# Optimization experiments

Measured on AMD Instinct MI355X. Metric: run time of the kernel, lower is better.

## Reference

```python
import jax, jax.numpy as jnp
import numpy as np

N_LAYERS = 6
D_MODEL = 512
D_FFN = 2048
N_STATE = 64
KSIZE = 31
BATCH = 8
SEQ = 2048
IN_SIZE = 80


def _ln(x, g, b, eps=1e-5):
    m = jnp.mean(x, axis=-1, keepdims=True)
    v = jnp.mean((x - m) ** 2, axis=-1, keepdims=True)
    return (x - m) * jax.lax.rsqrt(v + eps) * g + b


def _ffn(x, g, b, w1, b1, w2, b2):
    # LayerNorm -> Linear(D->F) -> GELU -> Linear(F->D)  (PositionalwiseFeedForward)
    h = jax.nn.gelu(_ln(x, g, b) @ w1 + b1)
    return h @ w2 + b2


def _dss(x, lam_re, lam_im, c_re, c_im, d_skip, log_dt, w_out, b_out):
    # Diagonal state-space (DSS-EXP): generate length-T kernel from diagonal poles,
    # apply causal conv via FFT, skip D*u, GELU, GLU output projection.
    Bx, T, H = x.shape
    dt = jnp.exp(log_dt)
    lam = -jnp.exp(lam_re) + 1j * lam_im                        # [N] stable poles (Re<0)
    P = jnp.exp(lam[:, None] * (dt * jnp.arange(T))[None, :])   # [N, T]
    C = c_re + 1j * c_im                                        # [H, N]
    kern = jnp.einsum('hn,nt->ht', C, P).real * dt              # [H, T]
    u = x.transpose(0, 2, 1)                                    # [B, H, T]
    n = 2 * T
    y = jnp.fft.irfft(jnp.fft.rfft(u, n=n) * jnp.fft.rfft(kern, n=n), n=n)[..., :T]
    y = y + d_skip[None, :, None] * u
    y = jax.nn.gelu(y.transpose(0, 2, 1))                       # [B, T, H]
    z = y @ w_out + b_out                                       # [B, T, 2H]
    a, g = jnp.split(z, 2, axis=-1)
    return a * jax.nn.sigmoid(g)                                # GLU


def _conv_module(x, g1, b1, bw, bb, dw, db, g2, b2, lw, lb):
    # LN -> 1x1 conv to 2D + GLU -> depthwise conv (SAME, k=31) -> LN -> GELU -> Linear
    y = _ln(x, g1, b1)
    y = y @ bw.T + bb                                           # [B, T, 2D]
    a, g = jnp.split(y, 2, axis=-1)
    y = a * jax.nn.sigmoid(g)                                   # GLU over channels
    yc = y.transpose(0, 2, 1)                                   # [B, D, T]
    yc = jax.lax.conv_general_dilated(
        yc, dw[:, None, :], (1,), 'SAME',
        feature_group_count=yc.shape[1],
        dimension_numbers=('NCH', 'OIH', 'NCH'))
    yc = yc + db[None, :, None]
    y = jax.nn.gelu(_ln(yc.transpose(0, 2, 1), g2, b2))
    return y @ lw.T + lb


def _forward(src, speaker_embs, src_w, src_b,
             ffn1_ln_g, ffn1_ln_b, ffn1_w1, ffn1_b1, ffn1_w2, ffn1_b2,
             norm1_g, norm1_b,
             lam_re, lam_im, c_re, c_im, ssm_d, log_dt, dss_out_w, dss_out_b,
             conv_ln_g, conv_ln_b, bneck_w, bneck_b, dw_w, dw_b,
             conv_ln2_g, conv_ln2_b, conv_lin_w, conv_lin_b,
             ffn2_ln_g, ffn2_ln_b, ffn2_w1, ffn2_b1, ffn2_w2, ffn2_b2,
             norm2_g, norm2_b, final_g, final_b):
    x = src @ src_w + src_b                                     # custom_src_module Linear
    for i in range(N_LAYERS):
        x = x + 0.5 * _ffn(x, ffn1_ln_g[i], ffn1_ln_b[i], ffn1_w1[i], ffn1_b1[i], ffn1_w2[i], ffn1_b2[i])
        skip = x
        x = _ln(x, norm1_g[i], norm1_b[i])
        x = _dss(x, lam_re[i], lam_im[i], c_re[i], c_im[i], ssm_d[i], log_dt[i], dss_out_w[i], dss_out_b[i])
        x = x + skip
        x = x + _conv_module(x, conv_ln_g[i], conv_ln_b[i], bneck_w[i], bneck_b[i], dw_w[i], dw_b[i],
                             conv_ln2_g[i], conv_ln2_b[i], conv_lin_w[i], conv_lin_b[i])
        x = _ln(x + 0.5 * _ffn(x, ffn2_ln_g[i], ffn2_ln_b[i], ffn2_w1[i], ffn2_b1[i], ffn2_w2[i], ffn2_b2[i]),
                norm2_g[i], norm2_b[i])
    x = _ln(x, final_g, final_b, eps=1e-6)
    return x + speaker_embs


def setup_inputs() -> dict:
    key = jax.random.key(0)
    ks = iter(jax.random.split(key, 64))
    def rn(shape, s=0.02):
        return (jax.random.normal(next(ks), shape) * s).astype(jnp.float32)
    L, D, F, N, K = N_LAYERS, D_MODEL, D_FFN, N_STATE, KSIZE
    return dict(
        src=jax.random.normal(next(ks), (BATCH, SEQ, IN_SIZE), dtype=jnp.float32),
        speaker_embs=jax.random.normal(next(ks), (BATCH, 1, D), dtype=jnp.float32),
        src_w=rn((IN_SIZE, D)), src_b=jnp.zeros((D,), jnp.float32),
        ffn1_ln_g=jnp.ones((L, D), jnp.float32), ffn1_ln_b=jnp.zeros((L, D), jnp.float32),
        ffn1_w1=rn((L, D, F)), ffn1_b1=jnp.zeros((L, F), jnp.float32),
        ffn1_w2=rn((L, F, D)), ffn1_b2=jnp.zeros((L, D), jnp.float32),
        norm1_g=jnp.ones((L, D), jnp.float32), norm1_b=jnp.zeros((L, D), jnp.float32),
        lam_re=rn((L, N), 0.5), lam_im=rn((L, N), 3.0),
        c_re=rn((L, D, N), 0.1), c_im=rn((L, D, N), 0.1),
        ssm_d=rn((L, D), 1.0), log_dt=jnp.full((L,), float(np.log(0.01)), jnp.float32),
        dss_out_w=rn((L, D, 2 * D)), dss_out_b=jnp.zeros((L, 2 * D), jnp.float32),
        conv_ln_g=jnp.ones((L, D), jnp.float32), conv_ln_b=jnp.zeros((L, D), jnp.float32),
        bneck_w=rn((L, 2 * D, D)), bneck_b=jnp.zeros((L, 2 * D), jnp.float32),
        dw_w=rn((L, D, K), 0.1), dw_b=jnp.zeros((L, D), jnp.float32),
        conv_ln2_g=jnp.ones((L, D), jnp.float32), conv_ln2_b=jnp.zeros((L, D), jnp.float32),
        conv_lin_w=rn((L, D, D)), conv_lin_b=jnp.zeros((L, D), jnp.float32),
        ffn2_ln_g=jnp.ones((L, D), jnp.float32), ffn2_ln_b=jnp.zeros((L, D), jnp.float32),
        ffn2_w1=rn((L, D, F)), ffn2_b1=jnp.zeros((L, F), jnp.float32),
        ffn2_w2=rn((L, F, D)), ffn2_b2=jnp.zeros((L, D), jnp.float32),
        norm2_g=jnp.ones((L, D), jnp.float32), norm2_b=jnp.zeros((L, D), jnp.float32),
        final_g=jnp.ones((D,), jnp.float32), final_b=jnp.zeros((D,), jnp.float32),
    )


def reference(src, speaker_embs, src_w, src_b,
              ffn1_ln_g, ffn1_ln_b, ffn1_w1, ffn1_b1, ffn1_w2, ffn1_b2,
              norm1_g, norm1_b,
              lam_re, lam_im, c_re, c_im, ssm_d, log_dt, dss_out_w, dss_out_b,
              conv_ln_g, conv_ln_b, bneck_w, bneck_b, dw_w, dw_b,
              conv_ln2_g, conv_ln2_b, conv_lin_w, conv_lin_b,
              ffn2_ln_g, ffn2_ln_b, ffn2_w1, ffn2_b1, ffn2_w2, ffn2_b2,
              norm2_g, norm2_b, final_g, final_b):
    return _forward(src, speaker_embs, src_w, src_b,
                    ffn1_ln_g, ffn1_ln_b, ffn1_w1, ffn1_b1, ffn1_w2, ffn1_b2,
                    norm1_g, norm1_b,
                    lam_re, lam_im, c_re, c_im, ssm_d, log_dt, dss_out_w, dss_out_b,
                    conv_ln_g, conv_ln_b, bneck_w, bneck_b, dw_w, dw_b,
                    conv_ln2_g, conv_ln2_b, conv_lin_w, conv_lin_b,
                    ffn2_ln_g, ffn2_ln_b, ffn2_w1, ffn2_b1, ffn2_w2, ffn2_b2,
                    norm2_g, norm2_b, final_g, final_b)
```

## Files before the change

### kernel.cpp

```cpp
#include <hip/hip_runtime.h>
#include <hip/hip_bf16.h>
#include <stdint.h>


#define NL 6
#define TT 2048
#define BB 8
#define DD 512
#define FF 2048
#define ROWS (BB*TT)

typedef __attribute__((ext_vector_type(4))) float f32x4;
typedef __attribute__((ext_vector_type(8))) short s16x8;

#define DEVI __device__ __forceinline__

DEVI float bf2f(uint32_t u) { union { uint32_t i; float f; } v; v.i = u << 16; return v.f; }
DEVI uint16_t f2bf(float f) {
    union { float f; uint32_t i; } v; v.f = f;
    uint32_t x = v.i;
    return (uint16_t)((x + 0x7fffu + ((x >> 16) & 1u)) >> 16);
}
DEVI float gelu_f(float x) {
    float x2 = x * x;
    float z  = x * fmaf(x2, 0.07135481627f, 1.5957691216f);
    return x * __builtin_amdgcn_rcpf(1.0f + __expf(-z));
}
DEVI float sigm(float x) { return __builtin_amdgcn_rcpf(1.0f + __expf(-x)); }

DEVI void gload16(const uint16_t* g, uint16_t* l) {
    __builtin_amdgcn_global_load_lds((const __attribute__((address_space(1))) void*)g,
                                     (__attribute__((address_space(3))) void*)l, 16, 0, 0);
}

__global__ void k_wtrans(const float* __restrict__ src, uint16_t* __restrict__ dst,
                         int K, int N) {
    __shared__ float tile[32][33];
    int l = blockIdx.z;
    const float* s = src + (size_t)l * K * N;
    uint16_t*    d = dst + (size_t)l * N * K;
    int n0 = blockIdx.x * 32, k0 = blockIdx.y * 32;
    int tx = threadIdx.x, ty = threadIdx.y;
#pragma unroll
    for (int i = 0; i < 4; i++) {
        int k = k0 + ty + i * 8;
        tile[ty + i * 8][tx] = s[(size_t)k * N + n0 + tx];
    }
    __syncthreads();
#pragma unroll
    for (int i = 0; i < 4; i++) {
        int n = n0 + ty + i * 8;
        d[(size_t)n * K + k0 + tx] = f2bf(tile[tx][ty + i * 8]);
    }
}
__global__ void k_wcvt(const float* __restrict__ src, uint16_t* __restrict__ dst, int n) {
    int i = blockIdx.x * 256 + threadIdx.x;
    if (i < n) dst[i] = f2bf(src[i]);
}
__global__ void k_dwt(const float* __restrict__ dw, float* __restrict__ dwt) {
    int i = blockIdx.x * 256 + threadIdx.x;
    int tot = NL * DD * 31;
    if (i >= tot) return;
    int l = i / (DD * 31), r = i % (DD * 31), d = r / 31, k = r % 31;
    dwt[(size_t)l * 31 * DD + k * DD + d] = dw[i];
}
__global__ void k_srcpad(const float* __restrict__ src, uint16_t* __restrict__ dst) {
    int i = blockIdx.x * 256 + threadIdx.x;
    if (i >= ROWS * 128) return;
    int r = i >> 7, c = i & 127;
    dst[i] = (c < 80) ? f2bf(src[(size_t)r * 80 + c]) : (uint16_t)0;
}
__global__ void k_wsrcpad(const float* __restrict__ w, uint16_t* __restrict__ dst) {
    int i = blockIdx.x * 256 + threadIdx.x;
    if (i >= DD * 128) return;
    int n = i >> 7, k = i & 127;
    dst[i] = (k < 80) ? f2bf(w[(size_t)k * DD + n]) : (uint16_t)0;
}

template <int MODE>
__global__ void k_ln(const float* __restrict__ in, void* __restrict__ outp,
                     const float* __restrict__ gam, const float* __restrict__ bet,
                     const float* __restrict__ spk, float eps) {
    int row  = blockIdx.x * 4 + (threadIdx.x >> 6);
    int lane = threadIdx.x & 63;
    const float* x = in + (size_t)row * DD;
    float4 a0 = *(const float4*)&x[lane * 4];
    float4 a1 = *(const float4*)&x[256 + lane * 4];
    float v[8] = {a0.x, a0.y, a0.z, a0.w, a1.x, a1.y, a1.z, a1.w};
    float s = 0.f, q = 0.f;
#pragma unroll
    for (int i = 0; i < 8; i++) { s += v[i]; q += v[i] * v[i]; }
#pragma unroll
    for (int m = 1; m < 64; m <<= 1) { s += __shfl_xor(s, m); q += __shfl_xor(q, m); }
    float mean = s * (1.0f / 512.0f);
    float var  = fmaxf(q * (1.0f / 512.0f) - mean * mean, 0.0f);
    float inv  = rsqrtf(var + eps);
    float4 g0 = *(const float4*)&gam[lane * 4];
    float4 g1 = *(const float4*)&gam[256 + lane * 4];
    float4 b0 = *(const float4*)&bet[lane * 4];
    float4 b1 = *(const float4*)&bet[256 + lane * 4];
    float gv[8] = {g0.x, g0.y, g0.z, g0.w, g1.x, g1.y, g1.z, g1.w};
    float bv[8] = {b0.x, b0.y, b0.z, b0.w, b1.x, b1.y, b1.z, b1.w};
    float y[8];
#pragma unroll
    for (int i = 0; i < 8; i++) y[i] = (v[i] - mean) * inv * gv[i] + bv[i];
    uint16_t* o = (uint16_t*)outp + (size_t)row * DD;
    uint2 p0, p1;
    p0.x = (uint32_t)f2bf(y[0]) | ((uint32_t)f2bf(y[1]) << 16);
    p0.y = (uint32_t)f2bf(y[2]) | ((uint32_t)f2bf(y[3]) << 16);
    p1.x = (uint32_t)f2bf(y[4]) | ((uint32_t)f2bf(y[5]) << 16);
    p1.y = (uint32_t)f2bf(y[6]) | ((uint32_t)f2bf(y[7]) << 16);
    *(uint2*)&o[lane * 4]       = p0;
    *(uint2*)&o[256 + lane * 4] = p1;
}

template <int M2>
__global__ void k_ln2(const float* __restrict__ in, float* __restrict__ X,
                      void* __restrict__ out2,
                      const float* __restrict__ g1, const float* __restrict__ b1,
                      const float* __restrict__ g2, const float* __restrict__ b2,
                      const float* __restrict__ spk, float eps2) {
    int row  = blockIdx.x * 4 + (threadIdx.x >> 6);
    int lane = threadIdx.x & 63;
    const float* x = in + (size_t)row * DD;
    float4 a0 = *(const float4*)&x[lane * 4];
    float4 a1 = *(const float4*)&x[256 + lane * 4];
    float v[8] = {a0.x, a0.y, a0.z, a0.w, a1.x, a1.y, a1.z, a1.w};
    float s = 0.f, q = 0.f;
#pragma unroll
    for (int i = 0; i < 8; i++) { s += v[i]; q += v[i] * v[i]; }
#pragma unroll
    for (int m = 1; m < 64; m <<= 1) { s += __shfl_xor(s, m); q += __shfl_xor(q, m); }
    float mean = s * (1.0f / 512.0f);
    float var  = fmaxf(q * (1.0f / 512.0f) - mean * mean, 0.0f);
    float inv  = rsqrtf(var + 1e-5f);
    float4 g0 = *(const float4*)&g1[lane * 4];
    float4 g1v = *(const float4*)&g1[256 + lane * 4];
    float4 b0 = *(const float4*)&b1[lane * 4];
    float4 b1v = *(const float4*)&b1[256 + lane * 4];
    float gv[8] = {g0.x, g0.y, g0.z, g0.w, g1v.x, g1v.y, g1v.z, g1v.w};
    float bv[8] = {b0.x, b0.y, b0.z, b0.w, b1v.x, b1v.y, b1v.z, b1v.w};
    float y[8];
    float s2 = 0.f, q2 = 0.f;
#pragma unroll
    for (int i = 0; i < 8; i++) {
        y[i] = (v[i] - mean) * inv * gv[i] + bv[i];
        s2 += y[i]; q2 += y[i] * y[i];
    }
    if (M2 == 6) {
        float* xo = X + (size_t)row * DD;
        *(float4*)&xo[lane * 4]       = make_float4(y[0], y[1], y[2], y[3]);
        *(float4*)&xo[256 + lane * 4] = make_float4(y[4], y[5], y[6], y[7]);
    }
#pragma unroll
    for (int m = 1; m < 64; m <<= 1) { s2 += __shfl_xor(s2, m); q2 += __shfl_xor(q2, m); }
    float mean2 = s2 * (1.0f / 512.0f);
    float var2  = fmaxf(q2 * (1.0f / 512.0f) - mean2 * mean2, 0.0f);
    float inv2  = rsqrtf(var2 + eps2);
    float4 G0 = *(const float4*)&g2[lane * 4];
    float4 G1 = *(const float4*)&g2[256 + lane * 4];
    float4 B0 = *(const float4*)&b2[lane * 4];
    float4 B1v = *(const float4*)&b2[256 + lane * 4];
    float Gv[8] = {G0.x, G0.y, G0.z, G0.w, G1.x, G1.y, G1.z, G1.w};
    float Bv[8] = {B0.x, B0.y, B0.z, B0.w, B1v.x, B1v.y, B1v.z, B1v.w};
    float z[8];
#pragma unroll
    for (int i = 0; i < 8; i++) z[i] = (y[i] - mean2) * inv2 * Gv[i] + Bv[i];
    if (M2 == 6) {
        uint16_t* o = (uint16_t*)out2 + (size_t)row * DD;
        uint2 p0, p1;
        p0.x = (uint32_t)f2bf(z[0]) | ((uint32_t)f2bf(z[1]) << 16);
        p0.y = (uint32_t)f2bf(z[2]) | ((uint32_t)f2bf(z[3]) << 16);
        p1.x = (uint32_t)f2bf(z[4]) | ((uint32_t)f2bf(z[5]) << 16);
        p1.y = (uint32_t)f2bf(z[6]) | ((uint32_t)f2bf(z[7]) << 16);
        *(uint2*)&o[lane * 4]       = p0;
        *(uint2*)&o[256 + lane * 4] = p1;
    } else {
        const float* sp = spk + (size_t)(row >> 11) * DD;
        float4 s0 = *(const float4*)&sp[lane * 4];
        float4 s1 = *(const float4*)&sp[256 + lane * 4];
        float* o = (float*)out2 + (size_t)row * DD;
        *(float4*)&o[lane * 4]       = make_float4(z[0]+s0.x, z[1]+s0.y, z[2]+s0.z, z[3]+s0.w);
        *(float4*)&o[256 + lane * 4] = make_float4(z[4]+s1.x, z[5]+s1.y, z[6]+s1.z, z[7]+s1.w);
    }
}

__global__ void k_gluln(const uint16_t* __restrict__ H, float* __restrict__ X,
                        uint16_t* __restrict__ out,
                        const float* __restrict__ gam, const float* __restrict__ bet) {
    int row  = blockIdx.x * 4 + (threadIdx.x >> 6);
    int lane = threadIdx.x & 63;
    const uint16_t* hr = H + (size_t)row * 1024;
    uint2 ha0 = *(const uint2*)&hr[lane * 4];
    uint2 ha1 = *(const uint2*)&hr[256 + lane * 4];
    uint2 hg0 = *(const uint2*)&hr[512 + lane * 4];
    uint2 hg1 = *(const uint2*)&hr[768 + lane * 4];
    uint32_t aw[4] = {ha0.x, ha0.y, ha1.x, ha1.y};
    uint32_t gw[4] = {hg0.x, hg0.y, hg1.x, hg1.y};
    float* xr = X + (size_t)row * DD;
    float4 x0 = *(const float4*)&xr[lane * 4];
    float4 x1 = *(const float4*)&xr[256 + lane * 4];
    float xv[8] = {x0.x, x0.y, x0.z, x0.w, x1.x, x1.y, x1.z, x1.w};
    float v[8];
#pragma unroll
    for (int p = 0; p < 4; p++) {
        float a0 = bf2f(aw[p] & 0xffffu), a1 = bf2f(aw[p] >> 16);
        float g0 = bf2f(gw[p] & 0xffffu), g1 = bf2f(gw[p] >> 16);
        v[2*p]   = xv[2*p]   + a0 * sigm(g0);
        v[2*p+1] = xv[2*p+1] + a1 * sigm(g1);
    }
    *(float4*)&xr[lane * 4]       = make_float4(v[0], v[1], v[2], v[3]);
    *(float4*)&xr[256 + lane * 4] = make_float4(v[4], v[5], v[6], v[7]);
    float s = 0.f, q = 0.f;
#pragma unroll
    for (int i = 0; i < 8; i++) { s += v[i]; q += v[i] * v[i]; }
#pragma unroll
    for (int m = 1; m < 64; m <<= 1) { s += __shfl_xor(s, m); q += __shfl_xor(q, m); }
    float mean = s * (1.0f / 512.0f);
    float var  = fmaxf(q * (1.0f / 512.0f) - mean * mean, 0.0f);
    float inv  = rsqrtf(var + 1e-5f);
    float4 g0 = *(const float4*)&gam[lane * 4];
    float4 g1 = *(const float4*)&gam[256 + lane * 4];
    float4 b0 = *(const float4*)&bet[lane * 4];
    float4 b1 = *(const float4*)&bet[256 + lane * 4];
    float gv[8] = {g0.x, g0.y, g0.z, g0.w, g1.x, g1.y, g1.z, g1.w};
    float bv[8] = {b0.x, b0.y, b0.z, b0.w, b1.x, b1.y, b1.z, b1.w};
    uint16_t* o = out + (size_t)row * DD;
    uint2 p0, p1;
    float y0 = (v[0]-mean)*inv*gv[0]+bv[0], y1 = (v[1]-mean)*inv*gv[1]+bv[1];
    float y2 = (v[2]-mean)*inv*gv[2]+bv[2], y3 = (v[3]-mean)*inv*gv[3]+bv[3];
    float y4 = (v[4]-mean)*inv*gv[4]+bv[4], y5 = (v[5]-mean)*inv*gv[5]+bv[5];
    float y6 = (v[6]-mean)*inv*gv[6]+bv[6], y7 = (v[7]-mean)*inv*gv[7]+bv[7];
    p0.x = (uint32_t)f2bf(y0) | ((uint32_t)f2bf(y1) << 16);
    p0.y = (uint32_t)f2bf(y2) | ((uint32_t)f2bf(y3) << 16);
    p1.x = (uint32_t)f2bf(y4) | ((uint32_t)f2bf(y5) << 16);
    p1.y = (uint32_t)f2bf(y6) | ((uint32_t)f2bf(y7) << 16);
    *(uint2*)&o[lane * 4]       = p0;
    *(uint2*)&o[256 + lane * 4] = p1;
}

template <int MODE, int BN>
__global__ __launch_bounds__(512, 2) void k_gemm3(
    const uint16_t* __restrict__ A, const uint16_t* __restrict__ Bt,
    const float* __restrict__ bias, int M, int N, int K,
    void* __restrict__ outp, float* __restrict__ X) {
    constexpr int MR = 8;
    constexpr int NR = BN / 64;
    constexpr int ABLK = 16;
    constexpr int BBLK = BN / 16;
    constexpr int APW = 2;
    constexpr int BPW = BBLK / 8;
    constexpr int LV  = APW + BPW;
    __shared__ __align__(16) uint16_t As[3][ABLK * 512];
    __shared__ __align__(16) uint16_t Bs[3][BBLK * 512];
    int tid = threadIdx.x;
    int wave = tid >> 6, lane = tid & 63;
    int l15 = lane & 15, l16 = lane >> 4;
    int wr = wave >> 2, wc = wave & 3;

    int nwg = gridDim.x;
    int q8  = nwg >> 3;
    int wg  = (blockIdx.x & 7) * q8 + (blockIdx.x >> 3);
    int nbx = M >> 8;
    int bx = wg % nbx, by = wg / nbx;
    int m0 = bx * 256, n0 = by * BN;

    const uint16_t* srcA[APW];
    const uint16_t* srcB[BPW];
#pragma unroll
    for (int p = 0; p < APW; p++) {
        int bi = wave * APW + p;
        srcA[p] = A + (size_t)(m0 + bi * 16 + l15) * K + l16 * 8;
    }
#pragma unroll
    for (int p = 0; p < BPW; p++) {
        int bi = wave * BPW + p;
        srcB[p] = Bt + (size_t)(n0 + bi * 16 + l15) * K + l16 * 8;
    }

    f32x4 acc[MR][NR];
#pragma unroll
    for (int i = 0; i < MR; i++)
#pragma unroll
        for (int j = 0; j < NR; j++) acc[i][j] = (f32x4){0.f, 0.f, 0.f, 0.f};

    auto STAGE = [&](int tt) {
        int b = tt % 3;
        int kof = tt << 5;
#pragma unroll
        for (int p = 0; p < APW; p++)
            gload16(srcA[p] + kof, &As[b][(wave * APW + p) * 512]);
#pragma unroll
        for (int p = 0; p < BPW; p++)
            gload16(srcB[p] + kof, &Bs[b][(wave * BPW + p) * 512]);
    };

    int nk = K >> 5;
    STAGE(0);
    STAGE(1);
    for (int t = 0; t < nk; ++t) {
        if (t + 1 < nk) {
            if (LV == 4) asm volatile("s_waitcnt vmcnt(4)" ::: "memory");
            else         asm volatile("s_waitcnt vmcnt(3)" ::: "memory");
        } else {
            asm volatile("s_waitcnt vmcnt(0)" ::: "memory");
        }
        __builtin_amdgcn_s_barrier();
        asm volatile("" ::: "memory");
        if (t + 2 < nk) STAGE(t + 2);
        int buf = t % 3;
        s16x8 af[MR], bfr[NR];
#pragma unroll
        for (int i = 0; i < MR; i++)
            af[i] = *(const s16x8*)&As[buf][(wr * MR + i) * 512 + lane * 8];
#pragma unroll
        for (int j = 0; j < NR; j++)
            bfr[j] = *(const s16x8*)&Bs[buf][(wc * NR + j) * 512 + lane * 8];
#pragma unroll
        for (int i = 0; i < MR; i++)
#pragma unroll
            for (int j = 0; j < NR; j++)
                acc[i][j] = __builtin_amdgcn_mfma_f32_16x16x32_bf16(af[i], bfr[j], acc[i][j], 0, 0, 0);
    }
#pragma unroll
    for (int i = 0; i < MR; i++) {
#pragma unroll
        for (int j = 0; j < NR; j++) {
            int gcol = n0 + wc * NR * 16 + j * 16 + l15;
            float bv = bias[gcol];
#pragma unroll
            for (int q = 0; q < 4; q++) {
                int grow = m0 + wr * MR * 16 + i * 16 + l16 * 4 + q;
                float v = acc[i][j][q] + bv;
                if (MODE == 0) {
                    ((uint16_t*)outp)[(size_t)grow * N + gcol] = f2bf(gelu_f(v));
                } else if (MODE == 1) {
                    ((uint16_t*)outp)[(size_t)grow * N + gcol] = f2bf(v);
                } else if (MODE == 2) {
                    X[(size_t)grow * DD + gcol] += 0.5f * v;
                } else if (MODE == 3) {
                    X[(size_t)grow * DD + gcol] += v;
                } else if (MODE == 4) {
                    ((float*)outp)[(size_t)grow * DD + gcol] =
                        X[(size_t)grow * DD + gcol] + 0.5f * v;
                } else {
                    X[(size_t)grow * DD + gcol] = v;
                }
            }
        }
    }
}

__global__ void k_tpose(const uint16_t* __restrict__ in, uint16_t* __restrict__ out,
                        int R, int C) {
    __shared__ uint16_t tile[32][33];
    size_t boff = (size_t)blockIdx.z * R * C;
    int c0 = blockIdx.x * 32, r0 = blockIdx.y * 32;
    int tx = threadIdx.x, ty = threadIdx.y;
#pragma unroll
    for (int i = 0; i < 4; i++)
        tile[ty + i * 8][tx] = in[boff + (size_t)(r0 + ty + i * 8) * C + c0 + tx];
    __syncthreads();
#pragma unroll
    for (int i = 0; i < 4; i++)
        out[boff + (size_t)(c0 + ty + i * 8) * R + r0 + tx] = tile[tx][ty + i * 8];
}

__global__ __launch_bounds__(64) void k_phiprep(
        const float* __restrict__ lam_re, const float* __restrict__ lam_im,
        const float* __restrict__ log_dt, uint16_t* __restrict__ PHI,
        float* __restrict__ A64f) {
    int l = blockIdx.x, n = threadIdx.x;
    float dt = expf(log_dt[l]);
    float lr = lam_re[l * 64 + n], li = lam_im[l * 64 + n];
    float mag = expf(-expf(lr) * dt), th = li * dt;
    float Are = mag * __cosf(th), Aim = mag * __sinf(th);
    float Pre = 1.f, Pim = 0.f;
    uint16_t* ph = PHI + (size_t)l * 8192;
    for (int tau = 0; tau < 64; tau++) {
        int s = 63 - tau;
        ph[n * 64 + s]        = f2bf(Pre);
        ph[(64 + n) * 64 + s] = f2bf(Pim);
        float nr = Pre * Are - Pim * Aim;
        float ni = Pre * Aim + Pim * Are;
        Pre = nr; Pim = ni;
    }
    A64f[l * 128 + 2 * n]     = Pre;
    A64f[l * 128 + 2 * n + 1] = Pim;
}

__global__ __launch_bounds__(64) void k_gprep(
        const float* __restrict__ lam_re, const float* __restrict__ lam_im,
        const float* __restrict__ c_re, const float* __restrict__ c_im,
        const float* __restrict__ ssm_d, const float* __restrict__ log_dt,
        int l, uint16_t* __restrict__ G) {
    int h = blockIdx.x, n = threadIdx.x;
    __shared__ float klds[64];
    float dt = expf(log_dt[l]);
    float lr = lam_re[l * 64 + n], li = lam_im[l * 64 + n];
    float mag = expf(-expf(lr) * dt), th = li * dt;
    float Are = mag * __cosf(th), Aim = mag * __sinf(th);
    float Cre = c_re[(size_t)l * DD * 64 + h * 64 + n];
    float Cim = c_im[(size_t)l * DD * 64 + h * 64 + n];
    uint16_t* Gh = G + (size_t)h * 64 * 192;
    float Pre = 1.f, Pim = 0.f;
    for (int r = 0; r < 64; r++) {
        float t = Cre * Pre - Cim * Pim;
        float s = t;
        s += __shfl_xor(s, 1);  s += __shfl_xor(s, 2);  s += __shfl_xor(s, 4);
        s += __shfl_xor(s, 8);  s += __shfl_xor(s, 16); s += __shfl_xor(s, 32);
        if (n == 0) klds[r] = dt * s;
        float nr = Pre * Are - Pim * Aim;
        float ni = Pre * Aim + Pim * Are;
        float wre = dt * (Cre * nr - Cim * ni);
        float wim = dt * (Cre * ni + Cim * nr);
        Gh[r * 192 + 64 + n]  = f2bf(wre);
        Gh[r * 192 + 128 + n] = f2bf(-wim);
        Pre = nr; Pim = ni;
    }
    __syncthreads();
    float dh = ssm_d[l * DD + h];
    for (int r = 0; r < 64; r++) {
        int c = n;
        float val = (c < r) ? klds[r - c] : (c == r ? klds[0] + dh : 0.f);
        Gh[r * 192 + c] = f2bf(val);
    }
}

__global__ __launch_bounds__(256) void k_pass1(
        const uint16_t* __restrict__ u, const uint16_t* __restrict__ PHI,
        uint16_t* __restrict__ E) {
    __shared__ __align__(16) uint16_t Phs[128 * 72];
    int tid = threadIdx.x;
    for (int v = tid; v < 1024; v += 256) {
        int row = v >> 3, kb = v & 7;
        *(s16x8*)&Phs[row * 72 + kb * 8] = *(const s16x8*)&PHI[row * 64 + kb * 8];
    }
    __syncthreads();
    int wave = tid >> 6, lane = tid & 63;
    int l15 = lane & 15, l16 = lane >> 4;
    int m0 = (wave & 1) * 64;
    int colbase = blockIdx.x * 128 + (wave >> 1) * 64;
    f32x4 acc[4][4];
#pragma unroll
    for (int i = 0; i < 4; i++)
#pragma unroll
        for (int j = 0; j < 4; j++) acc[i][j] = (f32x4){0.f, 0.f, 0.f, 0.f};
#pragma unroll
    for (int kt = 0; kt < 64; kt += 32) {
        s16x8 a[4], b[4];
#pragma unroll
        for (int i = 0; i < 4; i++)
            a[i] = *(const s16x8*)&Phs[(m0 + i * 16 + l15) * 72 + kt + l16 * 8];
#pragma unroll
        for (int j = 0; j < 4; j++)
            b[j] = *(const s16x8*)(u + (size_t)(colbase + j * 16 + l15) * 64 + kt + l16 * 8);
#pragma unroll
        for (int i = 0; i < 4; i++)
#pragma unroll
            for (int j = 0; j < 4; j++)
                acc[i][j] = __builtin_amdgcn_mfma_f32_16x16x32_bf16(a[i], b[j], acc[i][j], 0, 0, 0);
    }
#pragma unroll
    for (int i = 0; i < 4; i++)
#pragma unroll
        for (int j = 0; j < 4; j++) {
            int col = colbase + j * 16 + l15;
            int r0  = m0 + i * 16 + l16 * 4;
            uint32_t p0 = (uint32_t)f2bf(acc[i][j][0]) | ((uint32_t)f2bf(acc[i][j][1]) << 16);
            uint32_t p1 = (uint32_t)f2bf(acc[i][j][2]) | ((uint32_t)f2bf(acc[i][j][3]) << 16);
            *(uint2*)&E[(size_t)col * 128 + r0] = make_uint2(p0, p1);
        }
}

__global__ void k_pass2(const uint16_t* __restrict__ E, const float* __restrict__ A64f,
                        int l, uint16_t* __restrict__ Sp) {
    int gid = blockIdx.x * 256 + threadIdx.x;
    int n = gid & 63, bh = gid >> 6;
    int b = bh >> 9, h = bh & 511;
    float2 A = *(const float2*)&A64f[l * 128 + 2 * n];
    float Sre = 0.f, Sim = 0.f;
    const uint16_t* Eb = E + (size_t)bh * 32 * 128;
    uint16_t* So = Sp + (size_t)h * 32768 + (size_t)b * 32 * 128;
    for (int i = 0; i < 32; i++) {
        So[i * 128 + n]      = f2bf(Sre);
        So[i * 128 + 64 + n] = f2bf(Sim);
        float er = bf2f((uint32_t)Eb[i * 128 + n]);
        float ei = bf2f((uint32_t)Eb[i * 128 + 64 + n]);
        float nr = A.x * Sre - A.y * Sim + er;
        float ni = A.x * Sim + A.y * Sre + ei;
        Sre = nr; Sim = ni;
    }
}

__global__ __launch_bounds__(256) void k_pass3(
        const uint16_t* __restrict__ G, const uint16_t* __restrict__ u,
        const uint16_t* __restrict__ Sp, uint16_t* __restrict__ Y) {
    __shared__ __align__(16) uint16_t Gs[64 * 200];
    int h = blockIdx.x, tid = threadIdx.x;
    for (int v = tid; v < 1536; v += 256) {
        int row = v / 24, kb = v % 24;
        *(s16x8*)&Gs[row * 200 + kb * 8] = *(const s16x8*)&G[(size_t)h * 12288 + row * 192 + kb * 8];
    }
    __syncthreads();
    int wave = tid >> 6, lane = tid & 63;
    int l15 = lane & 15, l16 = lane >> 4;
    int wn = wave * 64;
    const uint16_t* uh = u + (size_t)h * TT;
    const uint16_t* sh = Sp + (size_t)h * 32768;
    f32x4 acc[4][4];
#pragma unroll
    for (int i = 0; i < 4; i++)
#pragma unroll
        for (int j = 0; j < 4; j++) acc[i][j] = (f32x4){0.f, 0.f, 0.f, 0.f};
#pragma unroll
    for (int kt = 0; kt < 192; kt += 32) {
        s16x8 a[4], b[4];
#pragma unroll
        for (int i = 0; i < 4; i++)
            a[i] = *(const s16x8*)&Gs[(i * 16 + l15) * 200 + kt + l16 * 8];
#pragma unroll
        for (int j = 0; j < 4; j++) {
            int col = wn + j * 16 + l15;
            const uint16_t* src;
            if (kt < 64)
                src = uh + (size_t)(col >> 5) * (DD * TT) + (col & 31) * 64 + kt + l16 * 8;
            else
                src = sh + (size_t)col * 128 + (kt - 64) + l16 * 8;
            b[j] = *(const s16x8*)src;
        }
#pragma unroll
        for (int i = 0; i < 4; i++)
#pragma unroll
            for (int j = 0; j < 4; j++)
                acc[i][j] = __builtin_amdgcn_mfma_f32_16x16x32_bf16(a[i], b[j], acc[i][j], 0, 0, 0);
    }
#pragma unroll
    for (int i = 0; i < 4; i++)
#pragma unroll
        for (int j = 0; j < 4; j++) {
            int col = wn + j * 16 + l15;
            int r0  = i * 16 + l16 * 4;
            uint16_t* dst = Y + (size_t)(col >> 5) * (DD * TT) + (size_t)h * TT + (col & 31) * 64 + r0;
            uint32_t p0 = (uint32_t)f2bf(acc[i][j][0]) | ((uint32_t)f2bf(acc[i][j][1]) << 16);
            uint32_t p1 = (uint32_t)f2bf(acc[i][j][2]) | ((uint32_t)f2bf(acc[i][j][3]) << 16);
            *(uint2*)&dst[0] = make_uint2(p0, p1);
        }
}

__global__ void k_tgelu(const uint16_t* __restrict__ y, uint16_t* __restrict__ out) {
    __shared__ uint16_t tile[32][33];
    int b = blockIdx.z;
    int t0 = blockIdx.x * 32, h0 = blockIdx.y * 32;
    int tx = threadIdx.x, ty = threadIdx.y;
    const uint16_t* yb = y + (size_t)b * DD * TT;
#pragma unroll
    for (int i = 0; i < 4; i++) {
        int h = h0 + ty + i * 8;
        tile[ty + i * 8][tx] = f2bf(gelu_f(bf2f((uint32_t)yb[(size_t)h * TT + t0 + tx])));
    }
    __syncthreads();
    uint16_t* ob = out + (size_t)b * TT * DD;
#pragma unroll
    for (int i = 0; i < 4; i++) {
        int t = t0 + ty + i * 8;
        ob[(size_t)t * DD + h0 + tx] = tile[tx][ty + i * 8];
    }
}

__global__ void k_glu(const uint16_t* __restrict__ z, uint16_t* __restrict__ out) {
    int i = blockIdx.x * 256 + threadIdx.x;
    int r = i >> 8;
    int c = (i & 255) * 2;
    uint32_t av = *(const uint32_t*)&z[(size_t)r * 1024 + c];
    uint32_t gv = *(const uint32_t*)&z[(size_t)r * 1024 + 512 + c];
    float a0 = bf2f(av & 0xffffu), a1 = bf2f(av >> 16);
    float g0 = bf2f(gv & 0xffffu), g1 = bf2f(gv >> 16);
    float v0 = a0 * sigm(g0), v1 = a1 * sigm(g1);
    uint32_t p = (uint32_t)f2bf(v0) | ((uint32_t)f2bf(v1) << 16);
    *(uint32_t*)&out[(size_t)r * DD + c] = p;
}

__global__ __launch_bounds__(256) void k_dwln(
        const uint16_t* __restrict__ in, const float* __restrict__ dwt,
        const float* __restrict__ db, const float* __restrict__ gam,
        const float* __restrict__ bet, uint16_t* __restrict__ out) {
    __shared__ __align__(16) uint16_t xs[34 * 512];
    __shared__ float red[4][4][2];
    int tid = threadIdx.x;
    int t0 = (blockIdx.x & 511) * 4;
    int b  = blockIdx.x >> 9;
    const uint16_t* ib = in + (size_t)b * TT * DD;
    for (int v = tid; v < 34 * 64; v += 256) {
        int row = v >> 6, seg = v & 63;
        int tj = t0 - 15 + row;
        uint4 val = make_uint4(0, 0, 0, 0);
        if (tj >= 0 && tj < TT) val = *(const uint4*)&ib[(size_t)tj * DD + seg * 8];
        *(uint4*)&xs[row * 512 + seg * 8] = val;
    }
    __syncthreads();
    int d = tid * 2;
    int wave = tid >> 6, lane = tid & 63;
    float a0[4], a1[4];
    float bv0 = db[d], bv1 = db[d + 1];
#pragma unroll
    for (int o = 0; o < 4; o++) { a0[o] = bv0; a1[o] = bv1; }
#pragma unroll
    for (int k = 0; k < 31; k++) {
        float2 w = *(const float2*)&dwt[k * DD + d];
#pragma unroll
        for (int o = 0; o < 4; o++) {
            uint32_t v = *(const uint32_t*)&xs[(o + k) * 512 + d];
            a0[o] = fmaf(bf2f(v & 0xffffu), w.x, a0[o]);
            a1[o] = fmaf(bf2f(v >> 16), w.y, a1[o]);
        }
    }
#pragma unroll
    for (int o = 0; o < 4; o++) {
        float ss = a0[o] + a1[o];
        float qq = a0[o] * a0[o] + a1[o] * a1[o];
#pragma unroll
        for (int m = 1; m < 64; m <<= 1) { ss += __shfl_xor(ss, m); qq += __shfl_xor(qq, m); }
        if (lane == 0) { red[o][wave][0] = ss; red[o][wave][1] = qq; }
    }
    __syncthreads();
    float g0 = gam[d], g1 = gam[d + 1], be0 = bet[d], be1 = bet[d + 1];
#pragma unroll
    for (int o = 0; o < 4; o++) {
        float s = red[o][0][0] + red[o][1][0] + red[o][2][0] + red[o][3][0];
        float q = red[o][0][1] + red[o][1][1] + red[o][2][1] + red[o][3][1];
        float mean = s * (1.0f / 512.0f);
        float var  = fmaxf(q * (1.0f / 512.0f) - mean * mean, 0.0f);
        float inv  = rsqrtf(var + 1e-5f);
        float y0 = gelu_f((a0[o] - mean) * inv * g0 + be0);
        float y1 = gelu_f((a1[o] - mean) * inv * g1 + be1);
        uint32_t p = (uint32_t)f2bf(y0) | ((uint32_t)f2bf(y1) << 16);
        *(uint32_t*)&out[((size_t)b * TT + t0 + o) * DD + d] = p;
    }
}

extern "C" void kernel_launch(void* const* d_in, const int* in_sizes, int n_in,
                              void* d_out, int out_size, void* d_ws, size_t ws_size,
                              hipStream_t stream) {
    const float* src        = (const float*)d_in[0];
    const float* speaker    = (const float*)d_in[1];
    const float* src_w      = (const float*)d_in[2];
    const float* src_b      = (const float*)d_in[3];
    const float* ffn1_ln_g  = (const float*)d_in[4];
    const float* ffn1_ln_b  = (const float*)d_in[5];
    const float* ffn1_w1    = (const float*)d_in[6];
    const float* ffn1_b1    = (const float*)d_in[7];
    const float* ffn1_w2    = (const float*)d_in[8];
    const float* ffn1_b2    = (const float*)d_in[9];
    const float* norm1_g    = (const float*)d_in[10];
    const float* norm1_b    = (const float*)d_in[11];
    const float* lam_re     = (const float*)d_in[12];
    const float* lam_im     = (const float*)d_in[13];
    const float* c_re       = (const float*)d_in[14];
    const float* c_im       = (const float*)d_in[15];
    const float* ssm_d      = (const float*)d_in[16];
    const float* log_dt     = (const float*)d_in[17];
    const float* dss_out_w  = (const float*)d_in[18];
    const float* dss_out_b  = (const float*)d_in[19];
    const float* conv_ln_g  = (const float*)d_in[20];
    const float* conv_ln_b  = (const float*)d_in[21];
    const float* bneck_w    = (const float*)d_in[22];
    const float* bneck_b    = (const float*)d_in[23];
    const float* dw_w       = (const float*)d_in[24];
    const float* dw_b       = (const float*)d_in[25];
    const float* conv_ln2_g = (const float*)d_in[26];
    const float* conv_ln2_b = (const float*)d_in[27];
    const float* conv_lin_w = (const float*)d_in[28];
    const float* conv_lin_b = (const float*)d_in[29];
    const float* ffn2_ln_g  = (const float*)d_in[30];
    const float* ffn2_ln_b  = (const float*)d_in[31];
    const float* ffn2_w1    = (const float*)d_in[32];
    const float* ffn2_b1    = (const float*)d_in[33];
    const float* ffn2_w2    = (const float*)d_in[34];
    const float* ffn2_b2    = (const float*)d_in[35];
    const float* norm2_g    = (const float*)d_in[36];
    const float* norm2_b    = (const float*)d_in[37];
    const float* final_g    = (const float*)d_in[38];
    const float* final_b    = (const float*)d_in[39];
    (void)in_sizes; (void)n_in; (void)out_size; (void)ws_size;

    uint8_t* ws = (uint8_t*)d_ws;
    float*    X   = (float*)   (ws + 0);
    float*    F0  = (float*)   (ws + 33554432);
    uint16_t* B1  = (uint16_t*)(ws + 67108864);
    uint16_t* B2  = (uint16_t*)(ws + 83886080);
    uint16_t* B3  = (uint16_t*)(ws + 100663296);
    uint16_t* H   = (uint16_t*)(ws + 117440512);
    uint16_t* Wf1a= (uint16_t*)(ws + 184549376);
    uint16_t* Wf1b= (uint16_t*)(ws + 197132288);
    uint16_t* Wds = (uint16_t*)(ws + 209715200);
    uint16_t* Wbn = (uint16_t*)(ws + 216006656);
    uint16_t* Wcl = (uint16_t*)(ws + 222298112);
    uint16_t* Wf2a= (uint16_t*)(ws + 225443840);
    uint16_t* Wf2b= (uint16_t*)(ws + 238026752);
    float*    DWT = (float*)   (ws + 250609664);
    uint16_t* PHI = (uint16_t*)(ws + 250990592);
    float*    A64f= (float*)   (ws + 251088896);

    uint16_t* GBUF = B1;
    uint16_t* SPK  = (uint16_t*)F0;
    uint16_t* EBUF = H;
    uint16_t* SRCB = B3;
    uint16_t* WSRC = B2;

    dim3 tb(32, 8);
    k_wtrans<<<dim3(FF/32, DD/32, NL), tb, 0, stream>>>(ffn1_w1, Wf1a, DD, FF);
    k_wtrans<<<dim3(DD/32, FF/32, NL), tb, 0, stream>>>(ffn1_w2, Wf1b, FF, DD);
    k_wtrans<<<dim3(1024/32, DD/32, NL), tb, 0, stream>>>(dss_out_w, Wds, DD, 1024);
    k_wcvt<<<(NL*1024*DD + 255)/256, 256, 0, stream>>>(bneck_w, Wbn, NL*1024*DD);
    k_wcvt<<<(NL*DD*DD + 255)/256, 256, 0, stream>>>(conv_lin_w, Wcl, NL*DD*DD);
    k_wtrans<<<dim3(FF/32, DD/32, NL), tb, 0, stream>>>(ffn2_w1, Wf2a, DD, FF);
    k_wtrans<<<dim3(DD/32, FF/32, NL), tb, 0, stream>>>(ffn2_w2, Wf2b, FF, DD);
    k_dwt<<<(NL*DD*31 + 255)/256, 256, 0, stream>>>(dw_w, DWT);
    k_phiprep<<<NL, 64, 0, stream>>>(lam_re, lam_im, log_dt, PHI, A64f);
    k_srcpad<<<(ROWS*128 + 255)/256, 256, 0, stream>>>(src, SRCB);
    k_wsrcpad<<<(DD*128 + 255)/256, 256, 0, stream>>>(src_w, WSRC);

    k_gemm3<5,128><<<256, 512, 0, stream>>>(SRCB, WSRC, src_b, ROWS, DD, 128, nullptr, X);
    k_ln<0><<<4096, 256, 0, stream>>>(X, B1, ffn1_ln_g, ffn1_ln_b, nullptr, 1e-5f);

    for (int l = 0; l < NL; l++) {
        k_gemm3<0,256><<<512, 512, 0, stream>>>(B1, Wf1a + (size_t)l*FF*DD, ffn1_b1 + l*FF,
                                                ROWS, FF, DD, H, nullptr);
        k_gemm3<2,128><<<256, 512, 0, stream>>>(H, Wf1b + (size_t)l*DD*FF, ffn1_b2 + l*DD,
                                                ROWS, DD, FF, nullptr, X);
        k_ln<0><<<4096, 256, 0, stream>>>(X, B1, norm1_g + l*DD, norm1_b + l*DD, nullptr, 1e-5f);
        k_tpose<<<dim3(DD/32, TT/32, BB), tb, 0, stream>>>(B1, B2, TT, DD);
        k_gprep<<<DD, 64, 0, stream>>>(lam_re, lam_im, c_re, c_im, ssm_d, log_dt, l, GBUF);
        k_pass1<<<1024, 256, 0, stream>>>(B2, PHI + (size_t)l*8192, EBUF);
        k_pass2<<<1024, 256, 0, stream>>>(EBUF, A64f, l, SPK);
        k_pass3<<<DD, 256, 0, stream>>>(GBUF, B2, SPK, B3);
        k_tgelu<<<dim3(TT/32, DD/32, BB), tb, 0, stream>>>(B3, B1);
        k_gemm3<1,256><<<256, 512, 0, stream>>>(B1, Wds + (size_t)l*1024*DD, dss_out_b + l*1024,
                                                ROWS, 1024, DD, H, nullptr);
        k_gluln<<<4096, 256, 0, stream>>>(H, X, B1, conv_ln_g + l*DD, conv_ln_b + l*DD);
        k_gemm3<1,256><<<256, 512, 0, stream>>>(B1, Wbn + (size_t)l*1024*DD, bneck_b + l*1024,
                                                ROWS, 1024, DD, H, nullptr);
        k_glu<<<ROWS, 256, 0, stream>>>(H, B2);
        k_dwln<<<BB*512, 256, 0, stream>>>(B2, DWT + (size_t)l*31*DD, dw_b + l*DD,
                                           conv_ln2_g + l*DD, conv_ln2_b + l*DD, B1);
        k_gemm3<3,128><<<256, 512, 0, stream>>>(B1, Wcl + (size_t)l*DD*DD, conv_lin_b + l*DD,
                                                ROWS, DD, DD, nullptr, X);
        k_ln<0><<<4096, 256, 0, stream>>>(X, B1, ffn2_ln_g + l*DD, ffn2_ln_b + l*DD, nullptr, 1e-5f);
        k_gemm3<0,256><<<512, 512, 0, stream>>>(B1, Wf2a + (size_t)l*FF*DD, ffn2_b1 + l*FF,
                                                ROWS, FF, DD, H, nullptr);
        k_gemm3<4,128><<<256, 512, 0, stream>>>(H, Wf2b + (size_t)l*DD*FF, ffn2_b2 + l*DD,
                                                ROWS, DD, FF, F0, X);
        if (l < NL - 1) {
            k_ln2<6><<<4096, 256, 0, stream>>>(F0, X, B1, norm2_g + l*DD, norm2_b + l*DD,
                                               ffn1_ln_g + (l+1)*DD, ffn1_ln_b + (l+1)*DD,
                                               nullptr, 1e-5f);
        } else {
            k_ln2<7><<<4096, 256, 0, stream>>>(F0, nullptr, d_out, norm2_g + l*DD, norm2_b + l*DD,
                                               final_g, final_b, speaker, 1e-6f);
        }
    }
}
```

Before: 3.657 ms.

## Deepen GEMM LDS pipeline to four stages and remap workgroup tile order

The main bf16 MFMA GEMM now keeps four LDS buffers in flight instead of three, prefetching three K-tiles ahead, with vmcnt waits adjusted to match. Launch bounds drop from two blocks per CU to one, since the larger LDS footprint would not fit two. The workgroup-to-tile mapping changes so each group of eight consecutive blocks covers a contiguous slice of M rows, aiming at better cache locality across XCDs. Transpose tiles are padded from 33 to 34 columns to change the LDS bank pattern. The cost is lower occupancy, which could hide less latency than the old two-blocks-per-CU setup.

```diff
diff --git a/kernel.cpp b/kernel.cpp
--- a/kernel.cpp
+++ b/kernel.cpp
@@ -240,7 +240,7 @@
 }
 
 template <int MODE, int BN>
-__global__ __launch_bounds__(512, 2) void k_gemm3(
+__global__ __launch_bounds__(512, 1) void k_gemm3(
     const uint16_t* __restrict__ A, const uint16_t* __restrict__ Bt,
     const float* __restrict__ bias, int M, int N, int K,
     void* __restrict__ outp, float* __restrict__ X) {
@@ -251,18 +251,18 @@
     constexpr int APW = 2;
     constexpr int BPW = BBLK / 8;
     constexpr int LV  = APW + BPW;
-    __shared__ __align__(16) uint16_t As[3][ABLK * 512];
-    __shared__ __align__(16) uint16_t Bs[3][BBLK * 512];
+    __shared__ __align__(16) uint16_t As[4][ABLK * 512];
+    __shared__ __align__(16) uint16_t Bs[4][BBLK * 512];
     int tid = threadIdx.x;
     int wave = tid >> 6, lane = tid & 63;
     int l15 = lane & 15, l16 = lane >> 4;
     int wr = wave >> 2, wc = wave & 3;
 
-    int nwg = gridDim.x;
-    int q8  = nwg >> 3;
-    int wg  = (blockIdx.x & 7) * q8 + (blockIdx.x >> 3);
-    int nbx = M >> 8;
-    int bx = wg % nbx, by = wg / nbx;
+    int nbx  = M >> 8;
+    int nbxq = nbx >> 3;
+    int x8 = blockIdx.x & 7, j = blockIdx.x >> 3;
+    int bx = x8 * nbxq + (j % nbxq);
+    int by = j / nbxq;
     int m0 = bx * 256, n0 = by * BN;
 
     const uint16_t* srcA[APW];
@@ -282,10 +282,10 @@
 #pragma unroll
     for (int i = 0; i < MR; i++)
 #pragma unroll
-        for (int j = 0; j < NR; j++) acc[i][j] = (f32x4){0.f, 0.f, 0.f, 0.f};
+        for (int j2 = 0; j2 < NR; j2++) acc[i][j2] = (f32x4){0.f, 0.f, 0.f, 0.f};
 
     auto STAGE = [&](int tt) {
-        int b = tt % 3;
+        int b = tt & 3;
         int kof = tt << 5;
 #pragma unroll
         for (int p = 0; p < APW; p++)
@@ -298,40 +298,46 @@
     int nk = K >> 5;
     STAGE(0);
     STAGE(1);
+    STAGE(2);
     for (int t = 0; t < nk; ++t) {
-        if (t + 1 < nk) {
-            if (LV == 4) asm volatile("s_waitcnt vmcnt(4)" ::: "memory");
-            else         asm volatile("s_waitcnt vmcnt(3)" ::: "memory");
+        int newer = nk - 1 - t;
+        if (newer > 2) newer = 2;
+        if (newer == 2) {
+            if constexpr (LV == 4) asm volatile("s_waitcnt vmcnt(8)" ::: "memory");
+            else                   asm volatile("s_waitcnt vmcnt(6)" ::: "memory");
+        } else if (newer == 1) {
+            if constexpr (LV == 4) asm volatile("s_waitcnt vmcnt(4)" ::: "memory");
+            else                   asm volatile("s_waitcnt vmcnt(3)" ::: "memory");
         } else {
             asm volatile("s_waitcnt vmcnt(0)" ::: "memory");
         }
         __builtin_amdgcn_s_barrier();
         asm volatile("" ::: "memory");
-        if (t + 2 < nk) STAGE(t + 2);
-        int buf = t % 3;
+        if (t + 3 < nk) STAGE(t + 3);
+        int buf = t & 3;
         s16x8 af[MR], bfr[NR];
 #pragma unroll
         for (int i = 0; i < MR; i++)
             af[i] = *(const s16x8*)&As[buf][(wr * MR + i) * 512 + lane * 8];
 #pragma unroll
-        for (int j = 0; j < NR; j++)
-            bfr[j] = *(const s16x8*)&Bs[buf][(wc * NR + j) * 512 + lane * 8];
+        for (int j2 = 0; j2 < NR; j2++)
+            bfr[j2] = *(const s16x8*)&Bs[buf][(wc * NR + j2) * 512 + lane * 8];
 #pragma unroll
         for (int i = 0; i < MR; i++)
 #pragma unroll
-            for (int j = 0; j < NR; j++)
-                acc[i][j] = __builtin_amdgcn_mfma_f32_16x16x32_bf16(af[i], bfr[j], acc[i][j], 0, 0, 0);
+            for (int j2 = 0; j2 < NR; j2++)
+                acc[i][j2] = __builtin_amdgcn_mfma_f32_16x16x32_bf16(af[i], bfr[j2], acc[i][j2], 0, 0, 0);
     }
 #pragma unroll
     for (int i = 0; i < MR; i++) {
 #pragma unroll
-        for (int j = 0; j < NR; j++) {
-            int gcol = n0 + wc * NR * 16 + j * 16 + l15;
+        for (int j2 = 0; j2 < NR; j2++) {
+            int gcol = n0 + wc * NR * 16 + j2 * 16 + l15;
             float bv = bias[gcol];
 #pragma unroll
             for (int q = 0; q < 4; q++) {
                 int grow = m0 + wr * MR * 16 + i * 16 + l16 * 4 + q;
-                float v = acc[i][j][q] + bv;
+                float v = acc[i][j2][q] + bv;
                 if (MODE == 0) {
                     ((uint16_t*)outp)[(size_t)grow * N + gcol] = f2bf(gelu_f(v));
                 } else if (MODE == 1) {
@@ -353,7 +359,7 @@
 
 __global__ void k_tpose(const uint16_t* __restrict__ in, uint16_t* __restrict__ out,
                         int R, int C) {
-    __shared__ uint16_t tile[32][33];
+    __shared__ uint16_t tile[32][34];
     size_t boff = (size_t)blockIdx.z * R * C;
     int c0 = blockIdx.x * 32, r0 = blockIdx.y * 32;
     int tx = threadIdx.x, ty = threadIdx.y;
@@ -549,7 +555,7 @@
 }
 
 __global__ void k_tgelu(const uint16_t* __restrict__ y, uint16_t* __restrict__ out) {
-    __shared__ uint16_t tile[32][33];
+    __shared__ uint16_t tile[32][34];
     int b = blockIdx.z;
     int t0 = blockIdx.x * 32, h0 = blockIdx.y * 32;
     int tx = threadIdx.x, ty = threadIdx.y;
```

Measured after the change: 3.594 ms. No clear change (-1.7%).
